# Performance work log

Measured on AMD Instinct MI355X. Metric: run time of the kernel, lower is better.

## Reference

```python
import jax, jax.numpy as jnp
import numpy as np

N_MODELS = 128
N_FEAT = 32
TREE_LAYERS = [64, 32, 16]
INPUT_SIZE = 512
BATCH = 8192
EPS = 1e-5


def _uniform(key, shape, fan_in, fan_out):
    stdv = np.sqrt(6.0 / (fan_in + fan_out))
    return jax.random.uniform(key, shape, jnp.float32, -stdv, stdv)


def setup_inputs() -> dict:
    key = jax.random.key(0)
    ks = jax.random.split(key, 8)
    x = jax.random.normal(ks[0], (BATCH, INPUT_SIZE), jnp.float32)
    # flattened per-tree feature indices, shape [n_models * n_feature]
    used_features = jax.random.randint(ks[1], (N_MODELS * N_FEAT,), 0, INPUT_SIZE, jnp.int32)
    W1 = _uniform(ks[2], (N_MODELS, N_FEAT, TREE_LAYERS[0]), N_FEAT, TREE_LAYERS[0])
    b1 = jnp.zeros((N_MODELS, 1, TREE_LAYERS[0]), jnp.float32)
    W2 = _uniform(ks[3], (N_MODELS, TREE_LAYERS[0], TREE_LAYERS[1]), TREE_LAYERS[0], TREE_LAYERS[1])
    b2 = jnp.zeros((N_MODELS, 1, TREE_LAYERS[1]), jnp.float32)
    W3 = _uniform(ks[4], (N_MODELS, TREE_LAYERS[1], TREE_LAYERS[2]), TREE_LAYERS[1], TREE_LAYERS[2])
    b3 = jnp.zeros((N_MODELS, 1, TREE_LAYERS[2]), jnp.float32)
    gamma1 = jnp.ones((N_MODELS * TREE_LAYERS[0],), jnp.float32)
    beta1 = jnp.zeros((N_MODELS * TREE_LAYERS[0],), jnp.float32)
    gamma2 = jnp.ones((N_MODELS * TREE_LAYERS[1],), jnp.float32)
    beta2 = jnp.zeros((N_MODELS * TREE_LAYERS[1],), jnp.float32)
    out_weight = jax.random.normal(ks[5], (N_MODELS * TREE_LAYERS[2], 1), jnp.float32)
    out_bias = jnp.zeros((1,), jnp.float32)
    return {
        "x": x, "used_features": used_features,
        "W1": W1, "b1": b1, "W2": W2, "b2": b2, "W3": W3, "b3": b3,
        "gamma1": gamma1, "beta1": beta1, "gamma2": gamma2, "beta2": beta2,
        "out_weight": out_weight, "out_bias": out_bias,
    }


def _batch_dense(h, W, b):
    # h: [B, n_models, in], W: [n_models, in, out], b: [n_models, 1, out]
    return jnp.einsum("bmi,mio->bmo", h, W) + b[None, :, 0, :]


def _batchnorm_train(z, gamma, beta):
    # BatchNorm1d in training mode over 2D input: per-feature batch stats (biased var)
    mean = jnp.mean(z, axis=0)
    var = jnp.var(z, axis=0)
    return (z - mean) * jax.lax.rsqrt(var + EPS) * gamma + beta


def reference(x, used_features, W1, b1, W2, b2, W3, b3,
              gamma1, beta1, gamma2, beta2, out_weight, out_bias):
    B = x.shape[0]
    # gather used features: [B, n_models * n_feature] -> [B, n_models, n_feature]
    h = x[:, used_features].reshape(B, N_MODELS, N_FEAT)
    # layer 1: grouped GEMM + BN + ReLU
    h = _batch_dense(h, W1, b1).reshape(B, -1)
    h = jax.nn.relu(_batchnorm_train(h, gamma1, beta1))
    # layer 2
    h = _batch_dense(h.reshape(B, N_MODELS, -1), W2, b2).reshape(B, -1)
    h = jax.nn.relu(_batchnorm_train(h, gamma2, beta2))
    # last layer (no BN/ReLU) -> pred
    pred = _batch_dense(h.reshape(B, N_MODELS, -1), W3, b3).reshape(B, -1)
    out = pred @ out_weight + out_bias
    return (out, pred)
```

## Files before the change

kernel.cpp:

```cpp
#include <hip/hip_runtime.h>
#include <hip/hip_bf16.h>

#define BATCH   8192
#define NM      128
#define NF      32
#define L1      64
#define L2O     32
#define L3O     16
#define INSZ    512
#define EPSV    1e-5f
#define CH      16
#define P64     64
#define GS1B    256
#define XS_STR  522
#define H1STR   80
#define H2STR   40

typedef __attribute__((ext_vector_type(8))) short short8;
typedef __attribute__((ext_vector_type(4))) float f32x4;

union U8 { short8 s8; unsigned u[4]; };

__device__ inline unsigned short f2bf(float f) {
    union { float f; unsigned u; } v; v.f = f;
    return (unsigned short)((v.u + 0x7FFF + ((v.u >> 16) & 1)) >> 16);
}
__device__ inline unsigned pkbf(float a, float b) {
    union { __hip_bfloat162 h; unsigned u; } c;
    c.h = __float22bfloat162_rn(float2{a, b});
    return c.u;
}

__global__ __launch_bounds__(256) void k_prep(
    const float* __restrict__ W1, const float* __restrict__ W2,
    const float* __restrict__ W3,
    unsigned short* __restrict__ W1p, unsigned short* __restrict__ W2p,
    unsigned short* __restrict__ W3p)
{
    int g = blockIdx.x*256 + threadIdx.x;
    int m = g / 4608, r = g % 4608;
    if (r < 2048) {
        int n = r >> 9, l = (r >> 3) & 63, s = r & 7;
        W1p[m*2048 + r] = f2bf(W1[m*2048 + ((l>>4)*8+s)*L1 + n*16 + (l&15)]);
    } else if (r < 4096) {
        int q = r - 2048;
        int f = q >> 9, l = (q >> 3) & 63, s = q & 7;
        int n2 = f >> 1, ks = f & 1;
        W2p[m*2048 + q] = f2bf(W2[m*2048 + (ks*32+(l>>4)*8+s)*L2O + n2*16 + (l&15)]);
    } else {
        int q = r - 4096;
        int l = (q >> 3) & 63, s = q & 7;
        W3p[m*512 + q] = f2bf(W3[m*512 + ((l>>4)*8+s)*L3O + (l&15)]);
    }
}

__global__ __launch_bounds__(512) void k_gs1(
    const float* __restrict__ x, const int* __restrict__ uf,
    const unsigned short* __restrict__ W1p,
    unsigned short* __restrict__ Ag,
    float* __restrict__ s1sum, float* __restrict__ s1sq)
{
    __shared__ unsigned short xs[32*XS_STR];
    __shared__ int sUf[NM*NF];
    const int blk = blockIdx.x, t = threadIdx.x;
    #pragma unroll
    for (int p = 0; p < 8; ++p) {
        const float4 v = *(const float4*)(x + (size_t)blk*32*INSZ + p*2048 + t*4);
        const int row = 4*p + (t>>7), col = (t&127)*4;
        *(unsigned*)(&xs[row*XS_STR + col])     = pkbf(v.x, v.y);
        *(unsigned*)(&xs[row*XS_STR + col + 2]) = pkbf(v.z, v.w);
    }
    #pragma unroll
    for (int p = 0; p < 2; ++p)
        ((int4*)sUf)[t + p*512] = ((const int4*)uf)[t + p*512];
    __syncthreads();

    const int w = t >> 6, l = t & 63, lr = l & 15, lg = l >> 4;
    const unsigned short* xr0 = xs + lr*XS_STR;
    const unsigned short* xr1 = xs + (16+lr)*XS_STR;
    for (int mi = 0; mi < 16; ++mi) {
        const int m = w*16 + mi;
        const int4 ia = ((const int4*)sUf)[m*8 + lg*2];
        const int4 ib = ((const int4*)sUf)[m*8 + lg*2 + 1];
        U8 A0, A1;
        A0.u[0] = xr0[ia.x] | ((unsigned)xr0[ia.y] << 16);
        A0.u[1] = xr0[ia.z] | ((unsigned)xr0[ia.w] << 16);
        A0.u[2] = xr0[ib.x] | ((unsigned)xr0[ib.y] << 16);
        A0.u[3] = xr0[ib.z] | ((unsigned)xr0[ib.w] << 16);
        A1.u[0] = xr1[ia.x] | ((unsigned)xr1[ia.y] << 16);
        A1.u[1] = xr1[ia.z] | ((unsigned)xr1[ia.w] << 16);
        A1.u[2] = xr1[ib.x] | ((unsigned)xr1[ib.y] << 16);
        A1.u[3] = xr1[ib.z] | ((unsigned)xr1[ib.w] << 16);
        *(short8*)(Ag + ((size_t)(blk*2  )*NM + m)*512 + lr*32 + lg*8) = A0.s8;
        *(short8*)(Ag + ((size_t)(blk*2+1)*NM + m)*512 + lr*32 + lg*8) = A1.s8;
        float sum[4], sq[4];
        #pragma unroll
        for (int n = 0; n < 4; ++n) {
            const short8 wf = *(const short8*)(W1p + m*2048 + n*512 + l*8);
            f32x4 z = {0.f,0.f,0.f,0.f};
            f32x4 c0 = __builtin_amdgcn_mfma_f32_16x16x32_bf16(A0.s8, wf, z, 0, 0, 0);
            f32x4 c1 = __builtin_amdgcn_mfma_f32_16x16x32_bf16(A1.s8, wf, z, 0, 0, 0);
            sum[n] = (c0[0]+c0[1]) + (c0[2]+c0[3]) + (c1[0]+c1[1]) + (c1[2]+c1[3]);
            sq[n]  = c0[0]*c0[0] + c0[1]*c0[1] + c0[2]*c0[2] + c0[3]*c0[3]
                   + c1[0]*c1[0] + c1[1]*c1[1] + c1[2]*c1[2] + c1[3]*c1[3];
        }
        #pragma unroll
        for (int n = 0; n < 4; ++n) {
            sum[n] += __shfl_xor(sum[n], 16); sum[n] += __shfl_xor(sum[n], 32);
            sq[n]  += __shfl_xor(sq[n], 16);  sq[n]  += __shfl_xor(sq[n], 32);
        }
        if (l < 16) {
            #pragma unroll
            for (int n = 0; n < 4; ++n) {
                s1sum[(size_t)blk*8192 + m*64 + n*16 + l] = sum[n];
                s1sq [(size_t)blk*8192 + m*64 + n*16 + l] = sq[n];
            }
        }
    }
}

__global__ __launch_bounds__(256) void k_fin(
    const float* __restrict__ sump, const float* __restrict__ sqp,
    const float* __restrict__ bias, const float* __restrict__ gamma,
    const float* __restrict__ beta, float* __restrict__ scale,
    float* __restrict__ shift, int nfeat, int parts, int slotMajor)
{
    int f = blockIdx.x*256 + threadIdx.x;
    if (f >= nfeat) return;
    float S = 0.f, Q = 0.f;
    if (slotMajor) {
        #pragma unroll 8
        for (int c = 0; c < parts; ++c) { S += sump[(size_t)c*nfeat + f]; Q += sqp[(size_t)c*nfeat + f]; }
    } else {
        #pragma unroll 8
        for (int c = 0; c < parts; ++c) { S += sump[(size_t)f*parts + c]; Q += sqp[(size_t)f*parts + c]; }
    }
    float mz   = S * (1.f/BATCH);
    float var  = Q * (1.f/BATCH) - mz*mz;
    float mean = mz + bias[f];
    float sc   = rsqrtf(var + EPSV) * gamma[f];
    scale[f] = sc; shift[f] = beta[f] - mean*sc;
}

__global__ __launch_bounds__(256) void k_stats2_p(
    const unsigned short* __restrict__ Ag, const unsigned short* __restrict__ W1p,
    const float* __restrict__ scale1, const float* __restrict__ shift1,
    const unsigned short* __restrict__ W2p,
    float* __restrict__ sum2p, float* __restrict__ sq2p)
{
    __shared__ unsigned short h1T[4][16*H1STR];
    const int m = blockIdx.x >> 4, chunk = blockIdx.x & 15;
    const int t = threadIdx.x, w = t >> 6, l = t & 63;
    const int lr = l & 15, lg = l >> 4;
    short8 w1f[4];
    #pragma unroll
    for (int n = 0; n < 4; ++n) w1f[n] = *(const short8*)(W1p + m*2048 + n*512 + l*8);
    short8 w2f[2][2];
    #pragma unroll
    for (int n2 = 0; n2 < 2; ++n2)
        #pragma unroll
        for (int ks = 0; ks < 2; ++ks)
            w2f[n2][ks] = *(const short8*)(W2p + m*2048 + (n2*2+ks)*512 + l*8);
    float4 sc1q[4], sh1q[4];
    #pragma unroll
    for (int n = 0; n < 4; ++n) {
        sc1q[n] = *(const float4*)(scale1 + m*L1 + n*16 + lg*4);
        sh1q[n] = *(const float4*)(shift1 + m*L1 + n*16 + lg*4);
    }
    unsigned short* hT = &h1T[w][0];
    float sumf[8] = {0,0,0,0,0,0,0,0}, sqf[8] = {0,0,0,0,0,0,0,0};
    for (int i = 0; i < 8; ++i) {
        const int rbG = chunk*32 + i*4 + w;
        const short8 a = *(const short8*)(Ag + ((size_t)rbG*NM + m)*512 + lr*32 + lg*8);
        #pragma unroll
        for (int n = 0; n < 4; ++n) {
            f32x4 z = {0.f,0.f,0.f,0.f};
            f32x4 acc = __builtin_amdgcn_mfma_f32_16x16x32_bf16(w1f[n], a, z, 0, 0, 0);
            float h0 = acc[0]*sc1q[n].x + sh1q[n].x; h0 = h0 > 0.f ? h0 : 0.f;
            float h1 = acc[1]*sc1q[n].y + sh1q[n].y; h1 = h1 > 0.f ? h1 : 0.f;
            float h2 = acc[2]*sc1q[n].z + sh1q[n].z; h2 = h2 > 0.f ? h2 : 0.f;
            float h3 = acc[3]*sc1q[n].w + sh1q[n].w; h3 = h3 > 0.f ? h3 : 0.f;
            uint2 pk; pk.x = pkbf(h0, h1); pk.y = pkbf(h2, h3);
            *(uint2*)(hT + lr*H1STR + n*16 + lg*4) = pk;
        }
        const short8 a20 = *(const short8*)(hT + lr*H1STR + lg*8);
        const short8 a21 = *(const short8*)(hT + lr*H1STR + 32 + lg*8);
        #pragma unroll
        for (int n2 = 0; n2 < 2; ++n2) {
            f32x4 z = {0.f,0.f,0.f,0.f};
            f32x4 acc = __builtin_amdgcn_mfma_f32_16x16x32_bf16(w2f[n2][0], a20, z, 0, 0, 0);
            acc = __builtin_amdgcn_mfma_f32_16x16x32_bf16(w2f[n2][1], a21, acc, 0, 0, 0);
            #pragma unroll
            for (int r = 0; r < 4; ++r) {
                sumf[n2*4+r] += acc[r];
                sqf [n2*4+r] += acc[r]*acc[r];
            }
        }
    }
    #pragma unroll
    for (int j = 0; j < 8; ++j) {
        #pragma unroll
        for (int mk = 1; mk < 16; mk <<= 1) {
            sumf[j] += __shfl_xor(sumf[j], mk);
            sqf[j]  += __shfl_xor(sqf[j], mk);
        }
    }
    if (lr == 0) {
        const int slot = chunk*4 + w;
        #pragma unroll
        for (int n2 = 0; n2 < 2; ++n2)
            #pragma unroll
            for (int r = 0; r < 4; ++r) {
                const int f = m*L2O + n2*16 + lg*4 + r;
                sum2p[(size_t)f*P64 + slot] = sumf[n2*4+r];
                sq2p [(size_t)f*P64 + slot] = sqf[n2*4+r];
            }
    }
}

__global__ __launch_bounds__(256) void k_final_p(
    const unsigned short* __restrict__ Ag, const unsigned short* __restrict__ W1p,
    const float* __restrict__ scale1, const float* __restrict__ shift1,
    const unsigned short* __restrict__ W2p,
    const float* __restrict__ scale2, const float* __restrict__ shift2,
    const unsigned short* __restrict__ W3p, const float* __restrict__ b3,
    const float* __restrict__ ow,
    float* __restrict__ pred, float* __restrict__ outpartT)
{
    __shared__ unsigned short h1T[4][16*H1STR];
    __shared__ unsigned short h2T[4][16*H2STR];
    const int m = blockIdx.x >> 4, chunk = blockIdx.x & 15;
    const int t = threadIdx.x, w = t >> 6, l = t & 63;
    const int lr = l & 15, lg = l >> 4;
    short8 w1f[4];
    #pragma unroll
    for (int n = 0; n < 4; ++n) w1f[n] = *(const short8*)(W1p + m*2048 + n*512 + l*8);
    short8 w2f[2][2];
    #pragma unroll
    for (int n2 = 0; n2 < 2; ++n2)
        #pragma unroll
        for (int ks = 0; ks < 2; ++ks)
            w2f[n2][ks] = *(const short8*)(W2p + m*2048 + (n2*2+ks)*512 + l*8);
    const short8 w3f = *(const short8*)(W3p + m*512 + l*8);
    float4 sc1q[4], sh1q[4];
    #pragma unroll
    for (int n = 0; n < 4; ++n) {
        sc1q[n] = *(const float4*)(scale1 + m*L1 + n*16 + lg*4);
        sh1q[n] = *(const float4*)(shift1 + m*L1 + n*16 + lg*4);
    }
    float4 sc2q[2], sh2q[2];
    #pragma unroll
    for (int n2 = 0; n2 < 2; ++n2) {
        sc2q[n2] = *(const float4*)(scale2 + m*L2O + n2*16 + lg*4);
        sh2q[n2] = *(const float4*)(shift2 + m*L2O + n2*16 + lg*4);
    }
    const float4 b3f = *(const float4*)(b3 + m*L3O + lg*4);
    const float4 owf = *(const float4*)(ow + m*L3O + lg*4);
    unsigned short* hT  = &h1T[w][0];
    unsigned short* hT2 = &h2T[w][0];
    for (int i = 0; i < 8; ++i) {
        const int rbG = chunk*32 + i*4 + w;
        const short8 a = *(const short8*)(Ag + ((size_t)rbG*NM + m)*512 + lr*32 + lg*8);
        #pragma unroll
        for (int n = 0; n < 4; ++n) {
            f32x4 z = {0.f,0.f,0.f,0.f};
            f32x4 acc = __builtin_amdgcn_mfma_f32_16x16x32_bf16(w1f[n], a, z, 0, 0, 0);
            float h0 = acc[0]*sc1q[n].x + sh1q[n].x; h0 = h0 > 0.f ? h0 : 0.f;
            float h1 = acc[1]*sc1q[n].y + sh1q[n].y; h1 = h1 > 0.f ? h1 : 0.f;
            float h2 = acc[2]*sc1q[n].z + sh1q[n].z; h2 = h2 > 0.f ? h2 : 0.f;
            float h3 = acc[3]*sc1q[n].w + sh1q[n].w; h3 = h3 > 0.f ? h3 : 0.f;
            uint2 pk; pk.x = pkbf(h0, h1); pk.y = pkbf(h2, h3);
            *(uint2*)(hT + lr*H1STR + n*16 + lg*4) = pk;
        }
        const short8 a20 = *(const short8*)(hT + lr*H1STR + lg*8);
        const short8 a21 = *(const short8*)(hT + lr*H1STR + 32 + lg*8);
        #pragma unroll
        for (int n2 = 0; n2 < 2; ++n2) {
            f32x4 z = {0.f,0.f,0.f,0.f};
            f32x4 acc = __builtin_amdgcn_mfma_f32_16x16x32_bf16(w2f[n2][0], a20, z, 0, 0, 0);
            acc = __builtin_amdgcn_mfma_f32_16x16x32_bf16(w2f[n2][1], a21, acc, 0, 0, 0);
            float h0 = acc[0]*sc2q[n2].x + sh2q[n2].x; h0 = h0 > 0.f ? h0 : 0.f;
            float h1 = acc[1]*sc2q[n2].y + sh2q[n2].y; h1 = h1 > 0.f ? h1 : 0.f;
            float h2 = acc[2]*sc2q[n2].z + sh2q[n2].z; h2 = h2 > 0.f ? h2 : 0.f;
            float h3 = acc[3]*sc2q[n2].w + sh2q[n2].w; h3 = h3 > 0.f ? h3 : 0.f;
            uint2 pk; pk.x = pkbf(h0, h1); pk.y = pkbf(h2, h3);
            *(uint2*)(hT2 + lr*H2STR + n2*16 + lg*4) = pk;
        }
        {
            const short8 a3 = *(const short8*)(hT2 + lr*H2STR + lg*8);
            f32x4 z = {0.f,0.f,0.f,0.f};
            f32x4 acc = __builtin_amdgcn_mfma_f32_16x16x32_bf16(w3f, a3, z, 0, 0, 0);
            float4 pv;
            pv.x = acc[0] + b3f.x; pv.y = acc[1] + b3f.y;
            pv.z = acc[2] + b3f.z; pv.w = acc[3] + b3f.w;
            const size_t row = (size_t)rbG*16 + lr;
            *(float4*)(pred + row*(NM*L3O) + m*L3O + lg*4) = pv;
            float v = pv.x*owf.x + pv.y*owf.y + pv.z*owf.z + pv.w*owf.w;
            v += __shfl_xor(v, 16); v += __shfl_xor(v, 32);
            if (l < 16) outpartT[(size_t)m*BATCH + rbG*16 + l] = v;
        }
    }
}

__global__ __launch_bounds__(256) void k_outT(
    const float* __restrict__ outpartT, const float* __restrict__ ob,
    float* __restrict__ out)
{
    int b = blockIdx.x*256 + threadIdx.x;
    float acc = ob[0];
    #pragma unroll 8
    for (int m = 0; m < NM; ++m) acc += outpartT[(size_t)m*BATCH + b];
    out[b] = acc;
}

__global__ __launch_bounds__(256) void k_gather(
    const float* __restrict__ x, const int* __restrict__ uf,
    unsigned short* __restrict__ Ag)
{
    __shared__ float xs[16*INSZ];
    __shared__ int   sUf[NM*NF];
    const int rb = blockIdx.x;
    const int t  = threadIdx.x;
    const float4* xsrc = (const float4*)(x + (size_t)rb*16*INSZ);
    float4* xdst = (float4*)xs;
    #pragma unroll
    for (int p = 0; p < 8; ++p) xdst[t + p*256] = xsrc[t + p*256];
    const int4* us = (const int4*)uf;
    int4* ud = (int4*)sUf;
    #pragma unroll
    for (int p = 0; p < 4; ++p) ud[t + p*256] = us[t + p*256];
    __syncthreads();
    unsigned* outp = (unsigned*)(Ag + (size_t)rb*NM*512);
    const int e = t*2, r = e >> 5, j = e & 31;
    for (int m = 0; m < NM; ++m) {
        const int i0 = sUf[m*NF + j], i1 = sUf[m*NF + j + 1];
        outp[m*256 + t] = pkbf(xs[r*INSZ + i0], xs[r*INSZ + i1]);
    }
}

__global__ __launch_bounds__(256) void k_stats1_m(
    const unsigned short* __restrict__ Ag, const unsigned short* __restrict__ W1p,
    float* __restrict__ sum1p, float* __restrict__ sq1p)
{
    const int m = blockIdx.x >> 4, chunk = blockIdx.x & 15;
    const int t = threadIdx.x, w = t >> 6, l = t & 63;
    const int lr = l & 15, lg = l >> 4;
    short8 w1f[4];
    #pragma unroll
    for (int n = 0; n < 4; ++n) w1f[n] = *(const short8*)(W1p + m*2048 + n*512 + l*8);
    float sum[4] = {0,0,0,0}, sq[4] = {0,0,0,0};
    for (int i = 0; i < 8; ++i) {
        const int rbG = chunk*32 + i*4 + w;
        const short8 a = *(const short8*)(Ag + ((size_t)rbG*NM + m)*512 + lr*32 + lg*8);
        #pragma unroll
        for (int n = 0; n < 4; ++n) {
            f32x4 acc = {0.f,0.f,0.f,0.f};
            acc = __builtin_amdgcn_mfma_f32_16x16x32_bf16(a, w1f[n], acc, 0, 0, 0);
            sum[n] += (acc[0]+acc[1]) + (acc[2]+acc[3]);
            sq[n]  += acc[0]*acc[0] + acc[1]*acc[1] + acc[2]*acc[2] + acc[3]*acc[3];
        }
    }
    #pragma unroll
    for (int n = 0; n < 4; ++n) {
        sum[n] += __shfl_xor(sum[n], 16); sum[n] += __shfl_xor(sum[n], 32);
        sq[n]  += __shfl_xor(sq[n], 16);  sq[n]  += __shfl_xor(sq[n], 32);
    }
    if (l < 16) {
        const int slot = chunk*4 + w;
        #pragma unroll
        for (int n = 0; n < 4; ++n) {
            const int f = m*L1 + n*16 + l;
            sum1p[(size_t)f*P64 + slot] = sum[n];
            sq1p [(size_t)f*P64 + slot] = sq[n];
        }
    }
}

extern "C" void kernel_launch(void* const* d_in, const int* in_sizes, int n_in,
                              void* d_out, int out_size, void* d_ws, size_t ws_size,
                              hipStream_t stream) {
    const float* x   = (const float*)d_in[0];
    const int*   uf  = (const int*  )d_in[1];
    const float* W1  = (const float*)d_in[2];
    const float* b1  = (const float*)d_in[3];
    const float* W2  = (const float*)d_in[4];
    const float* b2  = (const float*)d_in[5];
    const float* W3  = (const float*)d_in[6];
    const float* b3  = (const float*)d_in[7];
    const float* g1  = (const float*)d_in[8];
    const float* be1 = (const float*)d_in[9];
    const float* g2  = (const float*)d_in[10];
    const float* be2 = (const float*)d_in[11];
    const float* ow  = (const float*)d_in[12];
    const float* ob  = (const float*)d_in[13];

    float* out  = (float*)d_out;
    float* pred = out + BATCH;

    const size_t agElems = (size_t)BATCH * NM * NF;
    unsigned short* Ag  = (unsigned short*)d_ws;
    unsigned short* W1p = Ag + agElems;
    unsigned short* W2p = W1p + NM*2048;
    unsigned short* W3p = W2p + NM*2048;
    float* scale1 = (float*)(W3p + NM*512);
    float* shift1 = scale1 + NM*L1;
    float* scale2 = shift1 + NM*L1;
    float* shift2 = scale2 + NM*L2O;
    float* arena  = shift2 + NM*L2O;
    const size_t prefixBytes = (char*)arena - (char*)d_ws;

    const size_t arenaA = (size_t)GS1B*8192*4*2;
    const size_t s2Bytes = (size_t)NM*L2O*P64*4*2;
    const size_t needA = prefixBytes + arenaA;
    const size_t arenaB = (size_t)NM*L1*P64*4*2;
    (void)s2Bytes;

    k_prep<<<NM*4608/256, 256, 0, stream>>>(W1, W2, W3, W1p, W2p, W3p);

    if (ws_size >= needA) {
        float* s1sum = arena;
        float* s1sq  = s1sum + (size_t)GS1B*8192;
        float* s2sum = arena;
        float* s2sq  = s2sum + (size_t)NM*L2O*P64;
        float* outpartT = arena;

        k_gs1<<<GS1B, 512, 0, stream>>>(x, uf, W1p, Ag, s1sum, s1sq);
        k_fin<<<NM*L1/256, 256, 0, stream>>>(s1sum, s1sq, b1, g1, be1, scale1, shift1, NM*L1, GS1B, 1);
        k_stats2_p<<<NM*CH, 256, 0, stream>>>(Ag, W1p, scale1, shift1, W2p, s2sum, s2sq);
        k_fin<<<NM*L2O/256, 256, 0, stream>>>(s2sum, s2sq, b2, g2, be2, scale2, shift2, NM*L2O, P64, 0);
        k_final_p<<<NM*CH, 256, 0, stream>>>(Ag, W1p, scale1, shift1, W2p, scale2, shift2,
                                             W3p, b3, ow, pred, outpartT);
        k_outT<<<BATCH/256, 256, 0, stream>>>(outpartT, ob, out);
    } else {
        float* s1sum = arena;
        float* s1sq  = s1sum + (size_t)NM*L1*P64;
        float* outpartT = arena;
        float* s2sum = arena + arenaB/4;
        float* s2sq  = s2sum + (size_t)NM*L2O*P64;

        k_gather<<<BATCH/16, 256, 0, stream>>>(x, uf, Ag);
        k_stats1_m<<<NM*CH, 256, 0, stream>>>(Ag, W1p, s1sum, s1sq);
        k_fin<<<NM*L1/256, 256, 0, stream>>>(s1sum, s1sq, b1, g1, be1, scale1, shift1, NM*L1, P64, 0);
        k_stats2_p<<<NM*CH, 256, 0, stream>>>(Ag, W1p, scale1, shift1, W2p, s2sum, s2sq);
        k_fin<<<NM*L2O/256, 256, 0, stream>>>(s2sum, s2sq, b2, g2, be2, scale2, shift2, NM*L2O, P64, 0);
        k_final_p<<<NM*CH, 256, 0, stream>>>(Ag, W1p, scale1, shift1, W2p, scale2, shift2,
                                             W3p, b3, ow, pred, outpartT);
        k_outT<<<BATCH/256, 256, 0, stream>>>(outpartT, ob, out);
    }
}
```

Measured before the change: 115.4 us.

## Replace materialized gathered-feature buffer with bf16 x copy and on-the-fly gathers

Instead of writing a gathered, per-model bf16 activation buffer (BATCH*128*32 elements) in the first kernel and re-reading it in the two later passes, the first kernel now writes a compact bf16 copy of x (BATCH*512). The later kernels gather their A fragments directly from that copy using per-lane feature indices. This cuts global write and read traffic by a factor of about eight, at the cost of scattered 2-byte gather loads that rely on L2 and cache locality. It also folds the layer-3 bias into the MFMA accumulator init and removes the fallback small-workspace path.

```diff
diff --git a/kernel.cpp b/kernel.cpp
--- a/kernel.cpp
+++ b/kernel.cpp
@@ -57,7 +57,7 @@
 __global__ __launch_bounds__(512) void k_gs1(
     const float* __restrict__ x, const int* __restrict__ uf,
     const unsigned short* __restrict__ W1p,
-    unsigned short* __restrict__ Ag,
+    unsigned short* __restrict__ xbf,
     float* __restrict__ s1sum, float* __restrict__ s1sq)
 {
     __shared__ unsigned short xs[32*XS_STR];
@@ -67,8 +67,9 @@
     for (int p = 0; p < 8; ++p) {
         const float4 v = *(const float4*)(x + (size_t)blk*32*INSZ + p*2048 + t*4);
         const int row = 4*p + (t>>7), col = (t&127)*4;
-        *(unsigned*)(&xs[row*XS_STR + col])     = pkbf(v.x, v.y);
-        *(unsigned*)(&xs[row*XS_STR + col + 2]) = pkbf(v.z, v.w);
+        uint2 pk; pk.x = pkbf(v.x, v.y); pk.y = pkbf(v.z, v.w);
+        *(uint2*)(&xs[row*XS_STR + col]) = pk;
+        *(uint2*)(xbf + ((size_t)blk*32 + row)*INSZ + col) = pk;
     }
     #pragma unroll
     for (int p = 0; p < 2; ++p)
@@ -91,8 +92,6 @@
         A1.u[1] = xr1[ia.z] | ((unsigned)xr1[ia.w] << 16);
         A1.u[2] = xr1[ib.x] | ((unsigned)xr1[ib.y] << 16);
         A1.u[3] = xr1[ib.z] | ((unsigned)xr1[ib.w] << 16);
-        *(short8*)(Ag + ((size_t)(blk*2  )*NM + m)*512 + lr*32 + lg*8) = A0.s8;
-        *(short8*)(Ag + ((size_t)(blk*2+1)*NM + m)*512 + lr*32 + lg*8) = A1.s8;
         float sum[4], sq[4];
         #pragma unroll
         for (int n = 0; n < 4; ++n) {
@@ -142,8 +141,22 @@
     scale[f] = sc; shift[f] = beta[f] - mean*sc;
 }
 
-__global__ __launch_bounds__(256) void k_stats2_p(
-    const unsigned short* __restrict__ Ag, const unsigned short* __restrict__ W1p,
+__device__ __forceinline__ short8 gatherFrag(
+    const unsigned short* __restrict__ xbf, int rbG, int lr,
+    const int4 ia, const int4 ib)
+{
+    const unsigned short* xr = xbf + ((size_t)rbG*16 + lr)*INSZ;
+    U8 A;
+    A.u[0] = xr[ia.x] | ((unsigned)xr[ia.y] << 16);
+    A.u[1] = xr[ia.z] | ((unsigned)xr[ia.w] << 16);
+    A.u[2] = xr[ib.x] | ((unsigned)xr[ib.y] << 16);
+    A.u[3] = xr[ib.z] | ((unsigned)xr[ib.w] << 16);
+    return A.s8;
+}
+
+__global__ __launch_bounds__(256) void k_stats2g(
+    const unsigned short* __restrict__ xbf, const int* __restrict__ uf,
+    const unsigned short* __restrict__ W1p,
     const float* __restrict__ scale1, const float* __restrict__ shift1,
     const unsigned short* __restrict__ W2p,
     float* __restrict__ sum2p, float* __restrict__ sq2p)
@@ -152,6 +165,8 @@
     const int m = blockIdx.x >> 4, chunk = blockIdx.x & 15;
     const int t = threadIdx.x, w = t >> 6, l = t & 63;
     const int lr = l & 15, lg = l >> 4;
+    const int4 ia = ((const int4*)uf)[m*8 + lg*2];
+    const int4 ib = ((const int4*)uf)[m*8 + lg*2 + 1];
     short8 w1f[4];
     #pragma unroll
     for (int n = 0; n < 4; ++n) w1f[n] = *(const short8*)(W1p + m*2048 + n*512 + l*8);
@@ -171,7 +186,7 @@
     float sumf[8] = {0,0,0,0,0,0,0,0}, sqf[8] = {0,0,0,0,0,0,0,0};
     for (int i = 0; i < 8; ++i) {
         const int rbG = chunk*32 + i*4 + w;
-        const short8 a = *(const short8*)(Ag + ((size_t)rbG*NM + m)*512 + lr*32 + lg*8);
+        const short8 a = gatherFrag(xbf, rbG, lr, ia, ib);
         #pragma unroll
         for (int n = 0; n < 4; ++n) {
             f32x4 z = {0.f,0.f,0.f,0.f};
@@ -218,8 +233,9 @@
     }
 }
 
-__global__ __launch_bounds__(256) void k_final_p(
-    const unsigned short* __restrict__ Ag, const unsigned short* __restrict__ W1p,
+__global__ __launch_bounds__(256) void k_finalg(
+    const unsigned short* __restrict__ xbf, const int* __restrict__ uf,
+    const unsigned short* __restrict__ W1p,
     const float* __restrict__ scale1, const float* __restrict__ shift1,
     const unsigned short* __restrict__ W2p,
     const float* __restrict__ scale2, const float* __restrict__ shift2,
@@ -232,6 +248,8 @@
     const int m = blockIdx.x >> 4, chunk = blockIdx.x & 15;
     const int t = threadIdx.x, w = t >> 6, l = t & 63;
     const int lr = l & 15, lg = l >> 4;
+    const int4 ia = ((const int4*)uf)[m*8 + lg*2];
+    const int4 ib = ((const int4*)uf)[m*8 + lg*2 + 1];
     short8 w1f[4];
     #pragma unroll
     for (int n = 0; n < 4; ++n) w1f[n] = *(const short8*)(W1p + m*2048 + n*512 + l*8);
@@ -256,11 +274,12 @@
     }
     const float4 b3f = *(const float4*)(b3 + m*L3O + lg*4);
     const float4 owf = *(const float4*)(ow + m*L3O + lg*4);
+    f32x4 cb3; cb3[0] = b3f.x; cb3[1] = b3f.y; cb3[2] = b3f.z; cb3[3] = b3f.w;
     unsigned short* hT  = &h1T[w][0];
     unsigned short* hT2 = &h2T[w][0];
     for (int i = 0; i < 8; ++i) {
         const int rbG = chunk*32 + i*4 + w;
-        const short8 a = *(const short8*)(Ag + ((size_t)rbG*NM + m)*512 + lr*32 + lg*8);
+        const short8 a = gatherFrag(xbf, rbG, lr, ia, ib);
         #pragma unroll
         for (int n = 0; n < 4; ++n) {
             f32x4 z = {0.f,0.f,0.f,0.f};
@@ -288,11 +307,9 @@
         }
         {
             const short8 a3 = *(const short8*)(hT2 + lr*H2STR + lg*8);
-            f32x4 z = {0.f,0.f,0.f,0.f};
-            f32x4 acc = __builtin_amdgcn_mfma_f32_16x16x32_bf16(w3f, a3, z, 0, 0, 0);
+            f32x4 acc = __builtin_amdgcn_mfma_f32_16x16x32_bf16(w3f, a3, cb3, 0, 0, 0);
             float4 pv;
-            pv.x = acc[0] + b3f.x; pv.y = acc[1] + b3f.y;
-            pv.z = acc[2] + b3f.z; pv.w = acc[3] + b3f.w;
+            pv.x = acc[0]; pv.y = acc[1]; pv.z = acc[2]; pv.w = acc[3];
             const size_t row = (size_t)rbG*16 + lr;
             *(float4*)(pred + row*(NM*L3O) + m*L3O + lg*4) = pv;
             float v = pv.x*owf.x + pv.y*owf.y + pv.z*owf.z + pv.w*owf.w;
@@ -311,69 +328,6 @@
     #pragma unroll 8
     for (int m = 0; m < NM; ++m) acc += outpartT[(size_t)m*BATCH + b];
     out[b] = acc;
-}
-
-__global__ __launch_bounds__(256) void k_gather(
-    const float* __restrict__ x, const int* __restrict__ uf,
-    unsigned short* __restrict__ Ag)
-{
-    __shared__ float xs[16*INSZ];
-    __shared__ int   sUf[NM*NF];
-    const int rb = blockIdx.x;
-    const int t  = threadIdx.x;
-    const float4* xsrc = (const float4*)(x + (size_t)rb*16*INSZ);
-    float4* xdst = (float4*)xs;
-    #pragma unroll
-    for (int p = 0; p < 8; ++p) xdst[t + p*256] = xsrc[t + p*256];
-    const int4* us = (const int4*)uf;
-    int4* ud = (int4*)sUf;
-    #pragma unroll
-    for (int p = 0; p < 4; ++p) ud[t + p*256] = us[t + p*256];
-    __syncthreads();
-    unsigned* outp = (unsigned*)(Ag + (size_t)rb*NM*512);
-    const int e = t*2, r = e >> 5, j = e & 31;
-    for (int m = 0; m < NM; ++m) {
-        const int i0 = sUf[m*NF + j], i1 = sUf[m*NF + j + 1];
-        outp[m*256 + t] = pkbf(xs[r*INSZ + i0], xs[r*INSZ + i1]);
-    }
-}
-
-__global__ __launch_bounds__(256) void k_stats1_m(
-    const unsigned short* __restrict__ Ag, const unsigned short* __restrict__ W1p,
-    float* __restrict__ sum1p, float* __restrict__ sq1p)
-{
-    const int m = blockIdx.x >> 4, chunk = blockIdx.x & 15;
-    const int t = threadIdx.x, w = t >> 6, l = t & 63;
-    const int lr = l & 15, lg = l >> 4;
-    short8 w1f[4];
-    #pragma unroll
-    for (int n = 0; n < 4; ++n) w1f[n] = *(const short8*)(W1p + m*2048 + n*512 + l*8);
-    float sum[4] = {0,0,0,0}, sq[4] = {0,0,0,0};
-    for (int i = 0; i < 8; ++i) {
-        const int rbG = chunk*32 + i*4 + w;
-        const short8 a = *(const short8*)(Ag + ((size_t)rbG*NM + m)*512 + lr*32 + lg*8);
-        #pragma unroll
-        for (int n = 0; n < 4; ++n) {
-            f32x4 acc = {0.f,0.f,0.f,0.f};
-            acc = __builtin_amdgcn_mfma_f32_16x16x32_bf16(a, w1f[n], acc, 0, 0, 0);
-            sum[n] += (acc[0]+acc[1]) + (acc[2]+acc[3]);
-            sq[n]  += acc[0]*acc[0] + acc[1]*acc[1] + acc[2]*acc[2] + acc[3]*acc[3];
-        }
-    }
-    #pragma unroll
-    for (int n = 0; n < 4; ++n) {
-        sum[n] += __shfl_xor(sum[n], 16); sum[n] += __shfl_xor(sum[n], 32);
-        sq[n]  += __shfl_xor(sq[n], 16);  sq[n]  += __shfl_xor(sq[n], 32);
-    }
-    if (l < 16) {
-        const int slot = chunk*4 + w;
-        #pragma unroll
-        for (int n = 0; n < 4; ++n) {
-            const int f = m*L1 + n*16 + l;
-            sum1p[(size_t)f*P64 + slot] = sum[n];
-            sq1p [(size_t)f*P64 + slot] = sq[n];
-        }
-    }
 }
 
 extern "C" void kernel_launch(void* const* d_in, const int* in_sizes, int n_in,
@@ -397,54 +351,26 @@
     float* out  = (float*)d_out;
     float* pred = out + BATCH;
 
-    const size_t agElems = (size_t)BATCH * NM * NF;
-    unsigned short* Ag  = (unsigned short*)d_ws;
-    unsigned short* W1p = Ag + agElems;
+    unsigned short* W1p = (unsigned short*)d_ws;
     unsigned short* W2p = W1p + NM*2048;
     unsigned short* W3p = W2p + NM*2048;
-    float* scale1 = (float*)(W3p + NM*512);
+    unsigned short* xbf = W3p + NM*512;
+    float* scale1 = (float*)(xbf + (size_t)BATCH*INSZ);
     float* shift1 = scale1 + NM*L1;
     float* scale2 = shift1 + NM*L1;
     float* shift2 = scale2 + NM*L2O;
-    float* arena  = shift2 + NM*L2O;
-    const size_t prefixBytes = (char*)arena - (char*)d_ws;
-
-    const size_t arenaA = (size_t)GS1B*8192*4*2;
-    const size_t s2Bytes = (size_t)NM*L2O*P64*4*2;
-    const size_t needA = prefixBytes + arenaA;
-    const size_t arenaB = (size_t)NM*L1*P64*4*2;
-    (void)s2Bytes;
+    float* s1sum  = shift2 + NM*L2O;
+    float* s1sq   = s1sum + (size_t)GS1B*8192;
+    float* s2sum  = s1sq  + (size_t)GS1B*8192;
+    float* s2sq   = s2sum + (size_t)NM*L2O*P64;
+    float* outpartT = s2sq + (size_t)NM*L2O*P64;
 
     k_prep<<<NM*4608/256, 256, 0, stream>>>(W1, W2, W3, W1p, W2p, W3p);
-
-    if (ws_size >= needA) {
-        float* s1sum = arena;
-        float* s1sq  = s1sum + (size_t)GS1B*8192;
-        float* s2sum = arena;
-        float* s2sq  = s2sum + (size_t)NM*L2O*P64;
-        float* outpartT = arena;
-
-        k_gs1<<<GS1B, 512, 0, stream>>>(x, uf, W1p, Ag, s1sum, s1sq);
-        k_fin<<<NM*L1/256, 256, 0, stream>>>(s1sum, s1sq, b1, g1, be1, scale1, shift1, NM*L1, GS1B, 1);
-        k_stats2_p<<<NM*CH, 256, 0, stream>>>(Ag, W1p, scale1, shift1, W2p, s2sum, s2sq);
-        k_fin<<<NM*L2O/256, 256, 0, stream>>>(s2sum, s2sq, b2, g2, be2, scale2, shift2, NM*L2O, P64, 0);
-        k_final_p<<<NM*CH, 256, 0, stream>>>(Ag, W1p, scale1, shift1, W2p, scale2, shift2,
-                                             W3p, b3, ow, pred, outpartT);
-        k_outT<<<BATCH/256, 256, 0, stream>>>(outpartT, ob, out);
-    } else {
-        float* s1sum = arena;
-        float* s1sq  = s1sum + (size_t)NM*L1*P64;
-        float* outpartT = arena;
-        float* s2sum = arena + arenaB/4;
-        float* s2sq  = s2sum + (size_t)NM*L2O*P64;
-
-        k_gather<<<BATCH/16, 256, 0, stream>>>(x, uf, Ag);
-        k_stats1_m<<<NM*CH, 256, 0, stream>>>(Ag, W1p, s1sum, s1sq);
-        k_fin<<<NM*L1/256, 256, 0, stream>>>(s1sum, s1sq, b1, g1, be1, scale1, shift1, NM*L1, P64, 0);
-        k_stats2_p<<<NM*CH, 256, 0, stream>>>(Ag, W1p, scale1, shift1, W2p, s2sum, s2sq);
-        k_fin<<<NM*L2O/256, 256, 0, stream>>>(s2sum, s2sq, b2, g2, be2, scale2, shift2, NM*L2O, P64, 0);
-        k_final_p<<<NM*CH, 256, 0, stream>>>(Ag, W1p, scale1, shift1, W2p, scale2, shift2,
-                                             W3p, b3, ow, pred, outpartT);
-        k_outT<<<BATCH/256, 256, 0, stream>>>(outpartT, ob, out);
-    }
-}
+    k_gs1<<<GS1B, 512, 0, stream>>>(x, uf, W1p, xbf, s1sum, s1sq);
+    k_fin<<<NM*L1/256, 256, 0, stream>>>(s1sum, s1sq, b1, g1, be1, scale1, shift1, NM*L1, GS1B, 1);
+    k_stats2g<<<NM*CH, 256, 0, stream>>>(xbf, uf, W1p, scale1, shift1, W2p, s2sum, s2sq);
+    k_fin<<<NM*L2O/256, 256, 0, stream>>>(s2sum, s2sq, b2, g2, be2, scale2, shift2, NM*L2O, P64, 0);
+    k_finalg<<<NM*CH, 256, 0, stream>>>(xbf, uf, W1p, scale1, shift1, W2p, scale2, shift2,
+                                        W3p, b3, ow, pred, outpartT);
+    k_outT<<<BATCH/256, 256, 0, stream>>>(outpartT, ob, out);
+}
```

Measured after the change: 195.1 us. +69.0%, slower.
